# Performance work log

Measured on AMD Instinct MI355X. Metric: run time of the kernel, lower is better.

## Reference

```python
import jax, jax.numpy as jnp
import numpy as np

B, V, E = 64, 128, 8128  # batch, max_vertices, num candidate edges = V*(V-1)/2
VERTEX_W, EDGE_W, EXIST_W = 1.0, 1.0, 1.0


def setup_inputs() -> dict:
    key = jax.random.key(0)
    k = jax.random.split(key, 7)
    return {
        "pred_vertices": jax.random.normal(k[0], (B, V, 3), jnp.float32),
        "pred_existence": jax.random.uniform(k[1], (B, V), dtype=jnp.float32),
        "pred_edge_probs": jax.random.uniform(k[2], (B, E), dtype=jnp.float32),
        "target_vertices": jax.random.normal(k[3], (B, V, 3), jnp.float32),
        "target_existence": jax.random.randint(k[4], (B, V), 0, 2, jnp.int32),
        "edge_labels": jax.random.uniform(k[5], (B, E), dtype=jnp.float32),
        "vertex_counts": jax.random.randint(k[6], (B,), 1, V + 1, jnp.int32),
    }


def _lap(cost):
    """Exact O(n^3) Hungarian algorithm (Jonker-Volgenant style, row potentials)
    on a square float64 cost matrix. Returns rows[j] = row assigned to column j.
    Equivalent optimum to scipy.optimize.linear_sum_assignment."""
    n = cost.shape[0]
    INF = 1e18
    u = np.zeros(n + 1)
    v = np.zeros(n + 1)
    p = np.zeros(n + 1, dtype=np.int64)   # p[j] = row matched to column j (1-indexed)
    way = np.zeros(n + 1, dtype=np.int64)
    C = np.zeros((n + 1, n + 1))
    C[1:, 1:] = cost
    for i in range(1, n + 1):
        p[0] = i
        j0 = 0
        minv = np.full(n + 1, INF)
        used = np.zeros(n + 1, dtype=bool)
        while True:  # shortest augmenting path from row i
            used[j0] = True
            i0 = p[j0]
            cur = C[i0] - u[i0] - v
            free = ~used
            upd = free & (cur < minv)
            minv[upd] = cur[upd]
            way[upd] = j0
            masked = np.where(free, minv, INF)
            j0 = int(np.argmin(masked))
            delta = masked[j0]
            u[p[used]] += delta
            v[used] -= delta
            minv[free] -= delta
            if p[j0] == 0:
                break
        while j0 != 0:  # augment along the path
            j1 = way[j0]
            p[j0] = p[j1]
            j0 = j1
    return p[1:] - 1


def _match(pv, pe, tv, counts):
    """Per-sample Hungarian matching on detached host values (mirrors the
    original scipy linear_sum_assignment loop). counts[b] <= V so the cost
    matrix is square: [actual-target cols | dummy cols]. Returns flat
    (batch, pred, target) index triples for matches to real targets."""
    bs, mv = pv.shape[:2]
    bi, pi, ti = [], [], []
    for b in range(bs):
        c = int(counts[b])
        pos = np.abs(pv[b][:, None, :] - tv[b][:c][None, :, :]).sum(-1)  # [V,c] L1 cdist
        to_actual = pos + np.abs(pe[b] - 1.0)[:, None]                   # + existence-match cost
        to_dummy = np.repeat(pe[b][:, None], mv - c, axis=1)             # [V, V-c]
        cost = np.concatenate([to_actual, to_dummy], axis=1).astype(np.float64)
        rows = _lap(cost)
        # every column is matched; keep only columns pointing at real targets
        bi.append(np.full(c, b))
        pi.append(rows[:c])
        ti.append(np.arange(c))
    return np.concatenate(bi), np.concatenate(pi), np.concatenate(ti)


def _bce(p, t):
    # torch.nn.BCELoss (mean reduction), with log clamped at -100 like torch
    logp = jnp.maximum(jnp.log(p), -100.0)
    logq = jnp.maximum(jnp.log(1.0 - p), -100.0)
    return jnp.mean(-(t * logp + (1.0 - t) * logq))


def reference(pred_vertices, pred_existence, pred_edge_probs,
              target_vertices, target_existence, edge_labels, vertex_counts):
    bi, pi, ti = _match(np.asarray(pred_vertices), np.asarray(pred_existence),
                        np.asarray(target_vertices), np.asarray(vertex_counts))
    # SmoothL1 (beta=1) over matched pairs. Per-batch: mean over 3*k_b elems,
    # weighted by k_b, normalized by total matches => sum(elems)/3/total.
    d = jnp.abs(pred_vertices[bi, pi] - target_vertices[bi, ti])  # [M,3]
    sl1 = jnp.where(d < 1.0, 0.5 * d * d, d - 0.5)
    vertex_loss = sl1.sum() / (3.0 * bi.shape[0])
    existence_loss = _bce(pred_existence, target_existence.astype(jnp.float32))
    edge_loss = _bce(pred_edge_probs, edge_labels)  # min_edges == E for both
    total = VERTEX_W * vertex_loss + EXIST_W * existence_loss + EDGE_W * edge_loss
    return (total, vertex_loss, existence_loss, edge_loss)
```

## Files before the change

kernel.cpp:

```cpp
#include <hip/hip_runtime.h>
#include <math.h>

#define NB 64
#define NV 128
#define NEDGE_PER 8128
#define N_EDGE (NB * NEDGE_PER)
#define N_EX (NB * NV)
#define BID_ROUNDS 64
#define ARR_CAP 128


typedef unsigned long long u64;
typedef unsigned int uint2v __attribute__((ext_vector_type(2)));

__device__ __forceinline__ float sl1f(float d) {
    d = fabsf(d);
    return d < 1.0f ? 0.5f * d * d : d - 0.5f;
}
__device__ __forceinline__ unsigned umin2(unsigned a, unsigned b) { return a < b ? a : b; }


template <int CTRL>
__device__ __forceinline__ int dpp_i(int x) {
    return __builtin_amdgcn_update_dpp(0, x, CTRL, 0xF, 0xF, true);
}

__device__ __forceinline__ unsigned f2key(float x, int idx) {
    unsigned b = __float_as_uint(x);
    unsigned m = (unsigned)(((int)b) >> 31) | 0x80000000u;
    return ((b ^ m) & ~0xFFu) | (unsigned)idx;
}
__device__ __forceinline__ unsigned f2key_arr(float x, bool assigned, int idx) {
    unsigned b = __float_as_uint(x);
    unsigned m = (unsigned)(((int)b) >> 31) | 0x80000000u;
    return ((b ^ m) & ~0x1FFu) | (assigned ? 0x100u : 0u) | (unsigned)idx;
}
__device__ __forceinline__ unsigned bidkey(float b, int row) {
    return ((__float_as_uint(b) | 0x80000000u) & ~0xFFu) | (unsigned)row;
}

__device__ __forceinline__ unsigned wave_minkey32(unsigned k) {
    { unsigned o = (unsigned)dpp_i<0xB1>((int)k);  k = umin2(k, o); }
    { unsigned o = (unsigned)dpp_i<0x4E>((int)k);  k = umin2(k, o); }
    { unsigned o = (unsigned)dpp_i<0x141>((int)k); k = umin2(k, o); }
    { unsigned o = (unsigned)dpp_i<0x140>((int)k); k = umin2(k, o); }
#if __has_builtin(__builtin_amdgcn_permlane16_swap)
    { uint2v r = __builtin_amdgcn_permlane16_swap(k, k, false, false);
      k = umin2(k, umin2(r.x, r.y)); }
#else
    { k = umin2(k, (unsigned)__shfl_xor((int)k, 16)); }
#endif
#if __has_builtin(__builtin_amdgcn_permlane32_swap)
    { uint2v r = __builtin_amdgcn_permlane32_swap(k, k, false, false);
      k = umin2(k, umin2(r.x, r.y)); }
#else
    { k = umin2(k, (unsigned)__shfl_xor((int)k, 32)); }
#endif
    return k;
}

__device__ __forceinline__ void min2m(unsigned& k1, unsigned& k2, unsigned o1, unsigned o2) {
    if (k1 <= o1) {
        k2 = umin2(k2, o1);
    } else {
        k2 = umin2(o2, k1);
        k1 = o1;
    }
}
__device__ __forceinline__ void wave_min2_32(unsigned& k1, unsigned& k2) {
    { unsigned o1 = (unsigned)dpp_i<0xB1>((int)k1),  o2 = (unsigned)dpp_i<0xB1>((int)k2);  min2m(k1, k2, o1, o2); }
    { unsigned o1 = (unsigned)dpp_i<0x4E>((int)k1),  o2 = (unsigned)dpp_i<0x4E>((int)k2);  min2m(k1, k2, o1, o2); }
    { unsigned o1 = (unsigned)dpp_i<0x141>((int)k1), o2 = (unsigned)dpp_i<0x141>((int)k2); min2m(k1, k2, o1, o2); }
    { unsigned o1 = (unsigned)dpp_i<0x140>((int)k1), o2 = (unsigned)dpp_i<0x140>((int)k2); min2m(k1, k2, o1, o2); }
#if __has_builtin(__builtin_amdgcn_permlane16_swap)
    { uint2v r1 = __builtin_amdgcn_permlane16_swap(k1, k1, false, false);
      uint2v r2 = __builtin_amdgcn_permlane16_swap(k2, k2, false, false);
      min2m(k1, k2, r1.x, r2.x); min2m(k1, k2, r1.y, r2.y); }
#else
    { unsigned o1 = (unsigned)__shfl_xor((int)k1, 16), o2 = (unsigned)__shfl_xor((int)k2, 16); min2m(k1, k2, o1, o2); }
#endif
#if __has_builtin(__builtin_amdgcn_permlane32_swap)
    { uint2v r1 = __builtin_amdgcn_permlane32_swap(k1, k1, false, false);
      uint2v r2 = __builtin_amdgcn_permlane32_swap(k2, k2, false, false);
      min2m(k1, k2, r1.x, r2.x); min2m(k1, k2, r1.y, r2.y); }
#else
    { unsigned o1 = (unsigned)__shfl_xor((int)k1, 32), o2 = (unsigned)__shfl_xor((int)k2, 32); min2m(k1, k2, o1, o2); }
#endif
}

__device__ __forceinline__ int rl_i(int v, int sl) {
    return __builtin_amdgcn_readlane(v, sl);
}
__device__ __forceinline__ float rl_f(float v, int sl) {
    return __int_as_float(__builtin_amdgcn_readlane(__float_as_int(v), sl));
}



__global__ __launch_bounds__(64, 1) void hungarian_kernel(
    const float* __restrict__ pv,
    const float* __restrict__ pe,
    const float* __restrict__ tv,
    const int*   __restrict__ counts,
    double* __restrict__ ws_sl1)
{
    const int b = blockIdx.x;
    const int lane = threadIdx.x;
    const int c = counts[b];

    __shared__ float  s_costA[NV * 64];
    __shared__ float  s_costB[NV * 64];
    __shared__ float4 s_row[NV];
    __shared__ float  s_pe[NV];
    __shared__ float  s_v[NV];
    __shared__ float  s_u[NV];
    __shared__ int    s_x[NV];
    __shared__ float  s_rm1[NV], s_rm2[NV];
    __shared__ unsigned s_bid[NV];

    const float* pvb = pv + (size_t)b * NV * 3;
    const float* peb = pe + (size_t)b * NV;
    const float* tvb = tv + (size_t)b * NV * 3;

    {
        float x0 = pvb[lane * 3 + 0], y0 = pvb[lane * 3 + 1], z0 = pvb[lane * 3 + 2];
        float x1 = pvb[(lane + 64) * 3 + 0], y1 = pvb[(lane + 64) * 3 + 1], z1 = pvb[(lane + 64) * 3 + 2];
        float e0 = peb[lane], e1 = peb[lane + 64];
        s_row[lane]      = make_float4(x0, y0, z0, fabsf(e0 - 1.0f));
        s_row[lane + 64] = make_float4(x1, y1, z1, fabsf(e1 - 1.0f));
        s_pe[lane]       = e0;
        s_pe[lane + 64]  = e1;
    }
    const float tAx = tvb[lane * 3 + 0], tAy = tvb[lane * 3 + 1], tAz = tvb[lane * 3 + 2];
    const float tBx = tvb[(lane + 64) * 3 + 0], tBy = tvb[(lane + 64) * 3 + 1], tBz = tvb[(lane + 64) * 3 + 2];

    const int jA = lane + 1, jB = lane + 65;
    const int rA = lane + 1, rB = lane + 65;
    const bool realA = (jA <= c), realB = (jB <= c);

    __syncthreads();

    #pragma unroll 4
    for (int r = 0; r < NV; ++r) {
        float4 row = s_row[r];
        float per = s_pe[r];
        float cAv = realA ? (((fabsf(row.x - tAx) + fabsf(row.y - tAy)) + fabsf(row.z - tAz)) + row.w) : per;
        float cBv = realB ? (((fabsf(row.x - tBx) + fabsf(row.y - tBy)) + fabsf(row.z - tBz)) + row.w) : per;
        const int a = r * 64 + (lane ^ (r & 31));
        s_costA[a] = cAv;
        s_costB[a] = cBv;
    }
    __syncthreads();

    float bestA = 3.4e38f, bestB = 3.4e38f;
    #pragma unroll 4
    for (int r = 0; r < NV; ++r) {
        const int a = r * 64 + (lane ^ (r & 31));
        bestA = fminf(bestA, s_costA[a]);
        bestB = fminf(bestB, s_costB[a]);
    }
    float vA = bestA, vB = bestB;
    float uA = 0.0f, uB = 0.0f;
    int pA = 0, pB = 0;
    s_v[jA - 1] = vA; s_v[jB - 1] = vB;
    s_x[rA - 1] = 0;  s_x[rB - 1] = 0;
    s_u[rA - 1] = 0.0f; s_u[rB - 1] = 0.0f;

    int prevFree = NV + 1, stall = 0;
    for (int round = 0; round < BID_ROUNDS; ++round) {
        const int xAcur = s_x[rA - 1];
        const int xBcur = s_x[rB - 1];
        const u64 fA = __ballot(xAcur == 0);
        const u64 fB = __ballot(xBcur == 0);
        const int nfree = __popcll(fA) + __popcll(fB);
        if (nfree == 0 || nfree <= 8) break;
        if (nfree >= prevFree) { if (++stall >= 2) break; } else stall = 0;
        prevFree = nfree;

        s_bid[jA - 1] = 0u;
        s_bid[jB - 1] = 0u;

        #pragma unroll
        for (int half = 0; half < 2; ++half) {
            const int ri = (half == 0) ? rA : rB;
            const int xcur = (half == 0) ? xAcur : xBcur;
            if (xcur != 0) continue;
            const int r0 = ri - 1;
            const int swz = r0 & 31;
            float m1 = 3.4e38f, m2 = 3.4e38f;
            int j1 = 0, rot1 = 1000;
            #pragma unroll 4
            for (int j0 = 0; j0 < 64; ++j0) {
                const int a = r0 * 64 + (j0 ^ swz);
                float ca = s_costA[a] - s_v[j0];
                float cb = s_costB[a] - s_v[j0 + 64];
                int rotA = (j0 + 1 - ri) & 127;
                int rotB = (j0 + 65 - ri) & 127;
                if (ca < m1 || (ca == m1 && rotA < rot1)) { m2 = m1; m1 = ca; j1 = j0 + 1; rot1 = rotA; }
                else if (ca < m2) m2 = ca;
                if (cb < m1 || (cb == m1 && rotB < rot1)) { m2 = m1; m1 = cb; j1 = j0 + 65; rot1 = rotB; }
                else if (cb < m2) m2 = cb;
            }
            s_rm1[r0] = m1;
            s_rm2[r0] = m2;
            atomicMax(&s_bid[j1 - 1], bidkey(m2 - m1, ri));
        }

        {
            unsigned bk = s_bid[jA - 1];
            if (bk != 0u) {
                const int w = (int)(bk & 0xFFu);
                float m1w = s_rm1[w - 1], m2w = s_rm2[w - 1];
                vA -= (m2w - m1w);
                s_v[jA - 1] = vA;
                int old = pA; pA = w;
                s_x[w - 1] = jA;
                s_u[w - 1] = m2w;
                if (old) s_x[old - 1] = 0;
            }
        }
        {
            unsigned bk = s_bid[jB - 1];
            if (bk != 0u) {
                const int w = (int)(bk & 0xFFu);
                float m1w = s_rm1[w - 1], m2w = s_rm2[w - 1];
                vB -= (m2w - m1w);
                s_v[jB - 1] = vB;
                int old = pB; pB = w;
                s_x[w - 1] = jB;
                s_u[w - 1] = m2w;
                if (old) s_x[old - 1] = 0;
            }
        }
    }

    uA = s_u[rA - 1]; uB = s_u[rB - 1];
    u64 mA = __ballot(s_x[rA - 1] == 0);
    u64 mB = __ballot(s_x[rB - 1] == 0);
    u64 dA = 0ull, dB = 0ull;

    int steps = 0;
    while ((mA | mB) != 0ull && steps < ARR_CAP) {
        ++steps;
        const int i0 = mA ? (__builtin_ctzll(mA) + 1) : (__builtin_ctzll(mB) + 65);
        const bool hi = (i0 > 64);
        const int sl = (i0 - 1) & 63;
        const int ri0 = i0 - 1;
        const int a = ri0 * 64 + (lane ^ (ri0 & 31));

        const float rjA = s_costA[a] - vA;
        const float rjB = s_costB[a] - vB;

        unsigned k1 = f2key_arr(rjA, pA != 0, jA);
        unsigned k2 = f2key_arr(rjB, pB != 0, jB);
        if (k2 < k1) { unsigned t = k1; k1 = k2; k2 = t; }
        wave_min2_32(k1, k2);

        const int j1 = (int)(__builtin_amdgcn_readfirstlane(k1) & 0xFFu);
        const int j2 = (int)(__builtin_amdgcn_readfirstlane(k2) & 0xFFu);
        const bool h1 = (j1 > 64); const int s1 = (j1 - 1) & 63;
        const bool h2 = (j2 > 64); const int s2 = (j2 - 1) & 63;
        const float m1 = rl_f(h1 ? rjB : rjA, s1);
        const float m2 = rl_f(h2 ? rjB : rjA, s2);
        const int kdisp = rl_i(h1 ? pB : pA, s1);

        if (hi) mB &= ~(1ull << sl); else mA &= ~(1ull << sl);

        if (kdisp != 0 && !(m2 > m1)) {
            if (hi) dB |= (1ull << sl); else dA |= (1ull << sl);
            continue;
        }
        const float dlt = fmaxf(m2 - m1, 0.0f);
        if (jA == j1) { vA -= dlt; pA = i0; }
        if (jB == j1) { vB -= dlt; pB = i0; }
        if (rA == i0) { uA = m2; }
        if (rB == i0) { uB = m2; }
        if (kdisp != 0) {
            if (kdisp > 64) mB |= (1ull << (kdisp - 65)); else mA |= (1ull << (kdisp - 1));
        }
    }
    mA |= dA;
    mB |= dB;

    const float INF = 3.4e38f;
    while ((mA | mB) != 0ull) {
        const int f = mA ? (__builtin_ctzll(mA) + 1) : (__builtin_ctzll(mB) + 65);
        if (f <= 64) mA &= ~(1ull << (f - 1)); else mB &= ~(1ull << (f - 65));

        float minvA = INF, minvB = INF;
        int wayA = 0, wayB = 0;
        bool cuA = false, cuB = false;
        float SuseA = 0.0f, SuseB = 0.0f;
        bool rsA = (rA == f), rsB = (rB == f);
        float SsetA = 0.0f, SsetB = 0.0f;
        int j0 = 0;
        int i0 = f;
        float S = 0.0f;

        float u0 = rl_f((f > 64) ? uB : uA, (f - 1) & 63);
        float pre = u0;
        int ri0 = f - 1;
        int a = ri0 * 64 + (lane ^ (ri0 & 31));
        float cA = s_costA[a];
        float cB = s_costB[a];

        for (;;) {
            if (!cuA) { float cur = (cA - pre) - vA; if (cur < minvA) { minvA = cur; wayA = j0; } }
            if (!cuB) { float cur = (cB - pre) - vB; if (cur < minvB) { minvB = cur; wayB = j0; } }

            unsigned k = umin2(f2key(minvA, jA), f2key(minvB, jB));
            k = wave_minkey32(k);

            const int idx = (int)(__builtin_amdgcn_readfirstlane(k) & 0xFFu);
            const bool hij = (idx > 64);
            const int slj = (idx - 1) & 63;
            const float Snew = rl_f(hij ? minvB : minvA, slj);
            i0 = rl_i(hij ? pB : pA, slj);
            j0 = idx;

            if (jA == j0) { cuA = true; SuseA = Snew; minvA = INF; }
            if (jB == j0) { cuB = true; SuseB = Snew; minvB = INF; }
            S = Snew;
            if (i0 == 0) break;

            if (rA == i0) { rsA = true; SsetA = Snew; }
            if (rB == i0) { rsB = true; SsetB = Snew; }
            u0 = rl_f((i0 > 64) ? uB : uA, (i0 - 1) & 63);
            pre = u0 - S;
            ri0 = i0 - 1;
            a = ri0 * 64 + (lane ^ (ri0 & 31));
            cA = s_costA[a];
            cB = s_costB[a];
        }

        if (cuA) vA -= (S - SuseA);
        if (cuB) vB -= (S - SuseB);
        if (rsA) uA += (S - SsetA);
        if (rsB) uB += (S - SsetB);

        int j = j0;
        while (j != 0) {
            int j1 = rl_i((j <= 64) ? wayA : wayB, (j - 1) & 63);
            int pnew = (j1 == 0) ? f : rl_i((j1 <= 64) ? pA : pB, (j1 - 1) & 63);
            if (jA == j) pA = pnew;
            if (jB == j) pB = pnew;
            j = j1;
        }
    }

    double acc = 0.0;
    if (lane < c) {
        float4 prow = s_row[pA - 1];
        acc += (double)(sl1f(prow.x - tAx) + sl1f(prow.y - tAy) + sl1f(prow.z - tAz));
    }
    if (lane + 64 < c) {
        float4 prow = s_row[pB - 1];
        acc += (double)(sl1f(prow.x - tBx) + sl1f(prow.y - tBy) + sl1f(prow.z - tBz));
    }
    for (int off = 1; off < 64; off <<= 1) acc += __shfl_xor(acc, off);
    if (lane == 0) ws_sl1[b] = acc;
}


__device__ __forceinline__ double bce_term(float p, float t) {
    float logp = fmaxf(logf(p), -100.0f);
    float logq = fmaxf(logf(1.0f - p), -100.0f);
    return (double)(-(t * logp + (1.0f - t) * logq));
}

__global__ __launch_bounds__(256) void bce_exist_kernel(
    const float* __restrict__ pe, const int* __restrict__ te, double* __restrict__ out)
{
    const int tid = threadIdx.x;
    double acc = 0.0;
    for (int i = tid; i < N_EX; i += 256)
        acc += bce_term(pe[i], (float)te[i]);
    for (int off = 1; off < 64; off <<= 1) acc += __shfl_xor(acc, off);
    __shared__ double s[4];
    if ((tid & 63) == 0) s[tid >> 6] = acc;
    __syncthreads();
    if (tid == 0) out[0] = s[0] + s[1] + s[2] + s[3];
}

__global__ __launch_bounds__(256) void bce_edge_kernel(
    const float* __restrict__ p, const float* __restrict__ t, double* __restrict__ out)
{
    const int tid = threadIdx.x;
    double acc = 0.0;
    for (int i = blockIdx.x * 256 + tid; i < N_EDGE; i += 256 * 256)
        acc += bce_term(p[i], t[i]);
    for (int off = 1; off < 64; off <<= 1) acc += __shfl_xor(acc, off);
    __shared__ double s[4];
    if ((tid & 63) == 0) s[tid >> 6] = acc;
    __syncthreads();
    if (tid == 0) out[blockIdx.x] = s[0] + s[1] + s[2] + s[3];
}

__global__ __launch_bounds__(64) void finalize_kernel(
    const double* __restrict__ ws, const int* __restrict__ counts, float* __restrict__ out)
{
    const int lane = threadIdx.x;
    double vsum = ws[lane];
    double csum = (double)counts[lane];
    double edsum = 0.0;
    for (int k = lane; k < 256; k += 64) edsum += ws[128 + k];
    for (int off = 1; off < 64; off <<= 1) {
        vsum  += __shfl_xor(vsum, off);
        csum  += __shfl_xor(csum, off);
        edsum += __shfl_xor(edsum, off);
    }
    if (lane == 0) {
        double vloss  = vsum / (3.0 * csum);
        double eloss  = ws[64] / (double)N_EX;
        double edloss = edsum / (double)N_EDGE;
        double total  = vloss + eloss + edloss;
        out[0] = (float)total;
        out[1] = (float)vloss;
        out[2] = (float)eloss;
        out[3] = (float)edloss;
    }
}

extern "C" void kernel_launch(void* const* d_in, const int* in_sizes, int n_in,
                              void* d_out, int out_size, void* d_ws, size_t ws_size,
                              hipStream_t stream) {
    const float* pv     = (const float*)d_in[0];
    const float* pe     = (const float*)d_in[1];
    const float* pedge  = (const float*)d_in[2];
    const float* tv     = (const float*)d_in[3];
    const int*   te     = (const int*)d_in[4];
    const float* elab   = (const float*)d_in[5];
    const int*   counts = (const int*)d_in[6];
    double* ws = (double*)d_ws;
    float* out = (float*)d_out;

    hipLaunchKernelGGL(hungarian_kernel, dim3(NB), dim3(64), 0, stream, pv, pe, tv, counts, ws);
    hipLaunchKernelGGL(bce_exist_kernel, dim3(1), dim3(256), 0, stream, pe, te, ws + 64);
    hipLaunchKernelGGL(bce_edge_kernel, dim3(256), dim3(256), 0, stream, pedge, elab, ws + 128);
    hipLaunchKernelGGL(finalize_kernel, dim3(1), dim3(64), 0, stream, ws, counts, out);
}
```

Baseline: 654.1 us.

## Replace auction-style assignment phase with multi-source shortest augmenting paths

Result: slower. 918.7 us (+40.5%).

```diff
diff --git a/kernel.cpp b/kernel.cpp
--- a/kernel.cpp
+++ b/kernel.cpp
@@ -7,7 +7,6 @@
 #define N_EDGE (NB * NEDGE_PER)
 #define N_EX (NB * NV)
 #define BID_ROUNDS 64
-#define ARR_CAP 128
 
 
 typedef unsigned long long u64;
@@ -29,11 +28,6 @@
     unsigned b = __float_as_uint(x);
     unsigned m = (unsigned)(((int)b) >> 31) | 0x80000000u;
     return ((b ^ m) & ~0xFFu) | (unsigned)idx;
-}
-__device__ __forceinline__ unsigned f2key_arr(float x, bool assigned, int idx) {
-    unsigned b = __float_as_uint(x);
-    unsigned m = (unsigned)(((int)b) >> 31) | 0x80000000u;
-    return ((b ^ m) & ~0x1FFu) | (assigned ? 0x100u : 0u) | (unsigned)idx;
 }
 __device__ __forceinline__ unsigned bidkey(float b, int row) {
     return ((__float_as_uint(b) | 0x80000000u) & ~0xFFu) | (unsigned)row;
@@ -57,35 +51,6 @@
     { k = umin2(k, (unsigned)__shfl_xor((int)k, 32)); }
 #endif
     return k;
-}
-
-__device__ __forceinline__ void min2m(unsigned& k1, unsigned& k2, unsigned o1, unsigned o2) {
-    if (k1 <= o1) {
-        k2 = umin2(k2, o1);
-    } else {
-        k2 = umin2(o2, k1);
-        k1 = o1;
-    }
-}
-__device__ __forceinline__ void wave_min2_32(unsigned& k1, unsigned& k2) {
-    { unsigned o1 = (unsigned)dpp_i<0xB1>((int)k1),  o2 = (unsigned)dpp_i<0xB1>((int)k2);  min2m(k1, k2, o1, o2); }
-    { unsigned o1 = (unsigned)dpp_i<0x4E>((int)k1),  o2 = (unsigned)dpp_i<0x4E>((int)k2);  min2m(k1, k2, o1, o2); }
-    { unsigned o1 = (unsigned)dpp_i<0x141>((int)k1), o2 = (unsigned)dpp_i<0x141>((int)k2); min2m(k1, k2, o1, o2); }
-    { unsigned o1 = (unsigned)dpp_i<0x140>((int)k1), o2 = (unsigned)dpp_i<0x140>((int)k2); min2m(k1, k2, o1, o2); }
-#if __has_builtin(__builtin_amdgcn_permlane16_swap)
-    { uint2v r1 = __builtin_amdgcn_permlane16_swap(k1, k1, false, false);
-      uint2v r2 = __builtin_amdgcn_permlane16_swap(k2, k2, false, false);
-      min2m(k1, k2, r1.x, r2.x); min2m(k1, k2, r1.y, r2.y); }
-#else
-    { unsigned o1 = (unsigned)__shfl_xor((int)k1, 16), o2 = (unsigned)__shfl_xor((int)k2, 16); min2m(k1, k2, o1, o2); }
-#endif
-#if __has_builtin(__builtin_amdgcn_permlane32_swap)
-    { uint2v r1 = __builtin_amdgcn_permlane32_swap(k1, k1, false, false);
-      uint2v r2 = __builtin_amdgcn_permlane32_swap(k2, k2, false, false);
-      min2m(k1, k2, r1.x, r2.x); min2m(k1, k2, r1.y, r2.y); }
-#else
-    { unsigned o1 = (unsigned)__shfl_xor((int)k1, 32), o2 = (unsigned)__shfl_xor((int)k2, 32); min2m(k1, k2, o1, o2); }
-#endif
 }
 
 __device__ __forceinline__ int rl_i(int v, int sl) {
@@ -237,85 +202,52 @@
     uA = s_u[rA - 1]; uB = s_u[rB - 1];
     u64 mA = __ballot(s_x[rA - 1] == 0);
     u64 mB = __ballot(s_x[rB - 1] == 0);
-    u64 dA = 0ull, dB = 0ull;
-
-    int steps = 0;
-    while ((mA | mB) != 0ull && steps < ARR_CAP) {
-        ++steps;
-        const int i0 = mA ? (__builtin_ctzll(mA) + 1) : (__builtin_ctzll(mB) + 65);
-        const bool hi = (i0 > 64);
-        const int sl = (i0 - 1) & 63;
-        const int ri0 = i0 - 1;
-        const int a = ri0 * 64 + (lane ^ (ri0 & 31));
-
-        const float rjA = s_costA[a] - vA;
-        const float rjB = s_costB[a] - vB;
-
-        unsigned k1 = f2key_arr(rjA, pA != 0, jA);
-        unsigned k2 = f2key_arr(rjB, pB != 0, jB);
-        if (k2 < k1) { unsigned t = k1; k1 = k2; k2 = t; }
-        wave_min2_32(k1, k2);
-
-        const int j1 = (int)(__builtin_amdgcn_readfirstlane(k1) & 0xFFu);
-        const int j2 = (int)(__builtin_amdgcn_readfirstlane(k2) & 0xFFu);
-        const bool h1 = (j1 > 64); const int s1 = (j1 - 1) & 63;
-        const bool h2 = (j2 > 64); const int s2 = (j2 - 1) & 63;
-        const float m1 = rl_f(h1 ? rjB : rjA, s1);
-        const float m2 = rl_f(h2 ? rjB : rjA, s2);
-        const int kdisp = rl_i(h1 ? pB : pA, s1);
-
-        if (hi) mB &= ~(1ull << sl); else mA &= ~(1ull << sl);
-
-        if (kdisp != 0 && !(m2 > m1)) {
-            if (hi) dB |= (1ull << sl); else dA |= (1ull << sl);
-            continue;
-        }
-        const float dlt = fmaxf(m2 - m1, 0.0f);
-        if (jA == j1) { vA -= dlt; pA = i0; }
-        if (jB == j1) { vB -= dlt; pB = i0; }
-        if (rA == i0) { uA = m2; }
-        if (rB == i0) { uB = m2; }
-        if (kdisp != 0) {
-            if (kdisp > 64) mB |= (1ull << (kdisp - 65)); else mA |= (1ull << (kdisp - 1));
-        }
-    }
-    mA |= dA;
-    mB |= dB;
 
     const float INF = 3.4e38f;
     while ((mA | mB) != 0ull) {
-        const int f = mA ? (__builtin_ctzll(mA) + 1) : (__builtin_ctzll(mB) + 65);
-        if (f <= 64) mA &= ~(1ull << (f - 1)); else mB &= ~(1ull << (f - 65));
-
         float minvA = INF, minvB = INF;
         int wayA = 0, wayB = 0;
+        int srcA = 0, srcB = 0;
         bool cuA = false, cuB = false;
         float SuseA = 0.0f, SuseB = 0.0f;
-        bool rsA = (rA == f), rsB = (rB == f);
+        bool rsA = false, rsB = false;
         float SsetA = 0.0f, SsetB = 0.0f;
+
+        u64 fm = mA;
+        while (fm) {
+            const int f0 = __builtin_ctzll(fm); fm &= fm - 1;
+            const float u0 = rl_f(uA, f0);
+            const int a = f0 * 64 + (lane ^ (f0 & 31));
+            float ca = (s_costA[a] - u0) - vA;
+            float cb = (s_costB[a] - u0) - vB;
+            if (ca < minvA) { minvA = ca; wayA = 0; srcA = f0 + 1; }
+            if (cb < minvB) { minvB = cb; wayB = 0; srcB = f0 + 1; }
+        }
+        fm = mB;
+        while (fm) {
+            const int f0 = __builtin_ctzll(fm); fm &= fm - 1;
+            const float u0 = rl_f(uB, f0);
+            const int r0 = f0 + 64;
+            const int a = r0 * 64 + (lane ^ (r0 & 31));
+            float ca = (s_costA[a] - u0) - vA;
+            float cb = (s_costB[a] - u0) - vB;
+            if (ca < minvA) { minvA = ca; wayA = 0; srcA = f0 + 65; }
+            if (cb < minvB) { minvB = cb; wayB = 0; srcB = f0 + 65; }
+        }
+
         int j0 = 0;
-        int i0 = f;
         float S = 0.0f;
-
-        float u0 = rl_f((f > 64) ? uB : uA, (f - 1) & 63);
-        float pre = u0;
-        int ri0 = f - 1;
-        int a = ri0 * 64 + (lane ^ (ri0 & 31));
-        float cA = s_costA[a];
-        float cB = s_costB[a];
-
         for (;;) {
-            if (!cuA) { float cur = (cA - pre) - vA; if (cur < minvA) { minvA = cur; wayA = j0; } }
-            if (!cuB) { float cur = (cB - pre) - vB; if (cur < minvB) { minvB = cur; wayB = j0; } }
-
-            unsigned k = umin2(f2key(minvA, jA), f2key(minvB, jB));
+            unsigned kA2 = cuA ? 0xFFFFFFFFu : f2key(minvA, jA);
+            unsigned kB2 = cuB ? 0xFFFFFFFFu : f2key(minvB, jB);
+            unsigned k = umin2(kA2, kB2);
             k = wave_minkey32(k);
 
             const int idx = (int)(__builtin_amdgcn_readfirstlane(k) & 0xFFu);
             const bool hij = (idx > 64);
             const int slj = (idx - 1) & 63;
             const float Snew = rl_f(hij ? minvB : minvA, slj);
-            i0 = rl_i(hij ? pB : pA, slj);
+            const int i0 = rl_i(hij ? pB : pA, slj);
             j0 = idx;
 
             if (jA == j0) { cuA = true; SuseA = Snew; minvA = INF; }
@@ -325,12 +257,14 @@
 
             if (rA == i0) { rsA = true; SsetA = Snew; }
             if (rB == i0) { rsB = true; SsetB = Snew; }
-            u0 = rl_f((i0 > 64) ? uB : uA, (i0 - 1) & 63);
-            pre = u0 - S;
-            ri0 = i0 - 1;
-            a = ri0 * 64 + (lane ^ (ri0 & 31));
-            cA = s_costA[a];
-            cB = s_costB[a];
+            const float u0 = rl_f((i0 > 64) ? uB : uA, (i0 - 1) & 63);
+            const float pre = u0 - S;
+            const int ri0 = i0 - 1;
+            const int a = ri0 * 64 + (lane ^ (ri0 & 31));
+            const float cAr = s_costA[a];
+            const float cBr = s_costB[a];
+            if (!cuA) { float cur = (cAr - pre) - vA; if (cur < minvA) { minvA = cur; wayA = j0; } }
+            if (!cuB) { float cur = (cBr - pre) - vB; if (cur < minvB) { minvB = cur; wayB = j0; } }
         }
 
         if (cuA) vA -= (S - SuseA);
@@ -339,12 +273,21 @@
         if (rsB) uB += (S - SsetB);
 
         int j = j0;
-        while (j != 0) {
-            int j1 = rl_i((j <= 64) ? wayA : wayB, (j - 1) & 63);
-            int pnew = (j1 == 0) ? f : rl_i((j1 <= 64) ? pA : pB, (j1 - 1) & 63);
+        for (;;) {
+            const int jprev = rl_i((j <= 64) ? wayA : wayB, (j - 1) & 63);
+            if (jprev == 0) {
+                const int fsrc = rl_i((j <= 64) ? srcA : srcB, (j - 1) & 63);
+                if (jA == j) pA = fsrc;
+                if (jB == j) pB = fsrc;
+                if (rA == fsrc) uA += S;
+                if (rB == fsrc) uB += S;
+                if (fsrc > 64) mB &= ~(1ull << (fsrc - 65)); else mA &= ~(1ull << (fsrc - 1));
+                break;
+            }
+            const int pnew = rl_i((jprev <= 64) ? pA : pB, (jprev - 1) & 63);
             if (jA == j) pA = pnew;
             if (jB == j) pB = pnew;
-            j = j1;
+            j = jprev;
         }
     }
 
```

## Speculatively prefetch the runner-up column's cost row in the Hungarian search loop

Applied to the files above, without the earlier changes.

New measurement: 886.8 us. 1.36x slower.

```diff
diff --git a/kernel.cpp b/kernel.cpp
--- a/kernel.cpp
+++ b/kernel.cpp
@@ -294,7 +294,6 @@
         bool rsA = (rA == f), rsB = (rB == f);
         float SsetA = 0.0f, SsetB = 0.0f;
         int j0 = 0;
-        int i0 = f;
         float S = 0.0f;
 
         float u0 = rl_f((f > 64) ? uB : uA, (f - 1) & 63);
@@ -304,18 +303,25 @@
         float cA = s_costA[a];
         float cB = s_costB[a];
 
+        int pfCol = 0;
+        float pfCA = 0.0f, pfCB = 0.0f;
+
         for (;;) {
             if (!cuA) { float cur = (cA - pre) - vA; if (cur < minvA) { minvA = cur; wayA = j0; } }
             if (!cuB) { float cur = (cB - pre) - vB; if (cur < minvB) { minvB = cur; wayB = j0; } }
 
-            unsigned k = umin2(f2key(minvA, jA), f2key(minvB, jB));
-            k = wave_minkey32(k);
-
-            const int idx = (int)(__builtin_amdgcn_readfirstlane(k) & 0xFFu);
+            unsigned k1 = cuA ? 0xFFFFFFFFu : f2key(minvA, jA);
+            unsigned k2 = cuB ? 0xFFFFFFFFu : f2key(minvB, jB);
+            if (k2 < k1) { unsigned t = k1; k1 = k2; k2 = t; }
+            wave_min2_32(k1, k2);
+
+            const unsigned k1s = __builtin_amdgcn_readfirstlane(k1);
+            const unsigned k2s = __builtin_amdgcn_readfirstlane(k2);
+            const int idx = (int)(k1s & 0xFFu);
             const bool hij = (idx > 64);
             const int slj = (idx - 1) & 63;
             const float Snew = rl_f(hij ? minvB : minvA, slj);
-            i0 = rl_i(hij ? pB : pA, slj);
+            const int i0 = rl_i(hij ? pB : pA, slj);
             j0 = idx;
 
             if (jA == j0) { cuA = true; SuseA = Snew; minvA = INF; }
@@ -325,12 +331,29 @@
 
             if (rA == i0) { rsA = true; SsetA = Snew; }
             if (rB == i0) { rsB = true; SsetB = Snew; }
+
+            if (j0 == pfCol) {
+                cA = pfCA; cB = pfCB;
+            } else {
+                ri0 = i0 - 1;
+                a = ri0 * 64 + (lane ^ (ri0 & 31));
+                cA = s_costA[a];
+                cB = s_costB[a];
+            }
+            pfCol = 0;
+            const int idx2 = (int)(k2s & 0xFFu);
+            if (k2s != 0xFFFFFFFFu && idx2 >= 1 && idx2 <= NV && idx2 != j0) {
+                const int i2 = rl_i((idx2 > 64) ? pB : pA, (idx2 - 1) & 63);
+                if (i2 != 0) {
+                    const int ri2 = i2 - 1;
+                    const int a2 = ri2 * 64 + (lane ^ (ri2 & 31));
+                    pfCA = s_costA[a2];
+                    pfCB = s_costB[a2];
+                    pfCol = idx2;
+                }
+            }
             u0 = rl_f((i0 > 64) ? uB : uA, (i0 - 1) & 63);
             pre = u0 - S;
-            ri0 = i0 - 1;
-            a = ri0 * 64 + (lane ^ (ri0 & 31));
-            cA = s_costA[a];
-            cB = s_costB[a];
         }
 
         if (cuA) vA -= (S - SuseA);
```
